# Optimization experiments

Measured on AMD Instinct MI355X. Metric: run time of the kernel, lower is better.

The kernel has to match this reference:

```python
import jax, jax.numpy as jnp
import numpy as np

HEADS = 8

def setup_inputs() -> dict:
    key = jax.random.key(0)
    k1, k2, k3 = jax.random.split(key, 3)
    dim = 256
    B, H, W = 8, 128, 128
    x = jax.random.normal(k1, (B, dim, H, W), dtype=jnp.float32)
    w_qkv = jax.random.normal(k2, (3 * dim, dim), dtype=jnp.float32) * (1.0 / np.sqrt(dim))
    b_qkv = jnp.zeros((3 * dim,), dtype=jnp.float32)
    w_out = jax.random.normal(k3, (dim, dim), dtype=jnp.float32) * (1.0 / np.sqrt(dim))
    b_out = jnp.zeros((dim,), dtype=jnp.float32)
    return {"x": x, "w_qkv": w_qkv, "b_qkv": b_qkv, "w_out": w_out, "b_out": b_out}

def reference(x, w_qkv, b_qkv, w_out, b_out):
    B, C, H, W = x.shape
    hd = C // HEADS          # head dim
    N = H * W                # spatial tokens
    # 1x1 conv == channel matmul
    qkv = jnp.einsum('oc,bchw->bohw', w_qkv, x) + b_qkv[None, :, None, None]
    q, k, v = jnp.split(qkv, 3, axis=1)
    resh = lambda t: t.reshape(B, HEADS, hd, N)  # 'b (h c) h0 w0 -> b h c (h0 w0)'
    q = jax.nn.softmax(resh(q), axis=-2)  # softmax over channel dim
    k = jax.nn.softmax(resh(k), axis=-1)  # softmax over spatial dim
    v = resh(v)
    context = jnp.einsum('bhcn,bhdn->bhcd', k, v)   # [B,h,c,d]
    out = jnp.einsum('bhcd,bhcn->bhdn', context, q) # [B,h,d,N]
    out = out.reshape(B, C, H, W)
    out = jnp.einsum('oc,bchw->bohw', w_out, out) + b_out[None, :, None, None]
    return out
```

## Files before the change

kernel.cpp:

```cpp
#include <hip/hip_runtime.h>

#define NTOK 16384

typedef short           bf16x8 __attribute__((ext_vector_type(8)));
typedef float           f32x4  __attribute__((ext_vector_type(4)));
typedef unsigned short  u16x4  __attribute__((ext_vector_type(4)));

#define WHI_OFF 0
#define WLO_OFF 98304
#define CTX_OFF 196608
#define Z_OFF   262144
#define MHI_OFF 264192
#define MLO_OFF 526336

union UB8 { unsigned u[4]; bf16x8 v; };

#define GLL16(src, dst)                                                          \
    __builtin_amdgcn_global_load_lds(                                            \
        (const __attribute__((address_space(1))) unsigned*)(src),                \
        (__attribute__((address_space(3))) unsigned*)(dst), 16, 0, 0)

__device__ __forceinline__ void split2(float v0, float v1, unsigned& hi, unsigned& lo) {
    unsigned b0 = __float_as_uint(v0), b1 = __float_as_uint(v1);
    unsigned h0 = b0 & 0xffff0000u, h1 = b1 & 0xffff0000u;
    hi = (b0 >> 16) | h1;
    float r0 = v0 - __uint_as_float(h0);
    float r1 = v1 - __uint_as_float(h1);
    lo = (__float_as_uint(r0) >> 16) | (__float_as_uint(r1) & 0xffff0000u);
}

__device__ __forceinline__ unsigned short bf16_trunc(float v) {
    return (unsigned short)(__float_as_uint(v) >> 16);
}
__device__ __forceinline__ float bf16_f(unsigned short u) {
    return __uint_as_float(((unsigned)u) << 16);
}

__global__ void splitw_k(const float* __restrict__ w,
                         unsigned short* __restrict__ whi,
                         unsigned short* __restrict__ wlo)
{
    const int gid = blockIdx.x * 256 + threadIdx.x;
    const int row = gid >> 5, c8 = gid & 31;
    const float* wp = w + row * 256 + c8 * 8;
    float4 a = *(const float4*)wp;
    float4 b = *(const float4*)(wp + 4);
    uint4 hv, lv;
    split2(a.x, a.y, hv.x, lv.x);
    split2(a.z, a.w, hv.y, lv.y);
    split2(b.x, b.y, hv.z, lv.z);
    split2(b.z, b.w, hv.w, lv.w);
    const int didx = ((row >> 4) * 8 + (c8 >> 2)) * 64 + (c8 & 3) * 16 + (row & 15);
    ((uint4*)whi)[didx] = hv;
    ((uint4*)wlo)[didx] = lv;
}

__device__ __forceinline__ void loadA(const unsigned short* __restrict__ w,
                                      int tb0, int kblk, int lane, bf16x8 a[4])
{
#pragma unroll
    for (int rt = 0; rt < 4; ++rt)
        a[rt] = *(const bf16x8*)(w + (((tb0 + rt) * 8 + kblk) * 64 + lane) * 8);
}

__device__ __forceinline__ void stageX(const float* __restrict__ xb, int k0, int n0,
                                       float* __restrict__ xsbuf, int tid)
{
    const int r = tid >> 4, s = tid & 15;
    const float* src0 = xb + (size_t)(k0 + r) * NTOK + n0 + s * 4;
    char* lds_base = (char*)xsbuf + (tid >> 6) * 1024;
    GLL16(src0, lds_base);
    GLL16(src0 + (size_t)16 * NTOK, lds_base + 4096);
}

__device__ __forceinline__ void buildB(const float* __restrict__ xs,
                                       int quad, int l16, bf16x8 bh[4], bf16x8 bl[4])
{
#pragma unroll
    for (int ct = 0; ct < 4; ++ct) {
        UB8 hu, lu;
#pragma unroll
        for (int p = 0; p < 4; ++p) {
            float v0 = xs[(quad * 8 + 2 * p) * 64 + ct * 16 + l16];
            float v1 = xs[(quad * 8 + 2 * p + 1) * 64 + ct * 16 + l16];
            split2(v0, v1, hu.u[p], lu.u[p]);
        }
        bh[ct] = hu.v; bl[ct] = lu.v;
    }
}

__device__ __forceinline__ void mfma48(f32x4 acc[4][4],
                                       const bf16x8 ah[4], const bf16x8 al[4],
                                       const bf16x8 bh[4], const bf16x8 bl[4])
{
    __builtin_amdgcn_s_setprio(1);
#pragma unroll
    for (int rt = 0; rt < 4; ++rt)
#pragma unroll
        for (int ct = 0; ct < 4; ++ct) {
            acc[rt][ct] = __builtin_amdgcn_mfma_f32_16x16x32_bf16(ah[rt], bh[ct], acc[rt][ct], 0, 0, 0);
            acc[rt][ct] = __builtin_amdgcn_mfma_f32_16x16x32_bf16(al[rt], bh[ct], acc[rt][ct], 0, 0, 0);
            acc[rt][ct] = __builtin_amdgcn_mfma_f32_16x16x32_bf16(ah[rt], bl[ct], acc[rt][ct], 0, 0, 0);
        }
    __builtin_amdgcn_s_setprio(0);
}

__launch_bounds__(256, 2)
__global__ void kv_ctx_k(const float* __restrict__ x,
                         const unsigned short* __restrict__ whi,
                         const unsigned short* __restrict__ wlo,
                         const float* __restrict__ bqkv,
                         float* __restrict__ ctxn, float* __restrict__ zsum)
{
    __shared__ __align__(16) unsigned short kvt[32768];
    float* xs0 = (float*)((char*)kvt + 32768);
    float* xs1 = (float*)((char*)kvt + 40960);

    const int tid  = threadIdx.x;
    const int wave = tid >> 6, lane = tid & 63;
    const int quad = lane >> 4, l16 = lane & 15;
    const int b = blockIdx.x >> 6, tile = blockIdx.x & 63;
    const float* xb = x + (size_t)b * 256 * NTOK;

    f32x4 cacc[2][2][2];
#pragma unroll
    for (int a0 = 0; a0 < 2; ++a0)
#pragma unroll
        for (int a1 = 0; a1 < 2; ++a1)
#pragma unroll
            for (int a2 = 0; a2 < 2; ++a2)
                cacc[a0][a1][a2] = (f32x4){0.f, 0.f, 0.f, 0.f};
    float zacc = 0.f;

    for (int chunk = 0; chunk < 4; ++chunk) {
        const int n0 = tile * 256 + chunk * 64;

        for (int half = 0; half < 2; ++half) {
            f32x4 acc[4][4];
#pragma unroll
            for (int rt = 0; rt < 4; ++rt)
#pragma unroll
                for (int ct = 0; ct < 4; ++ct) acc[rt][ct] = (f32x4){0.f, 0.f, 0.f, 0.f};

            const int tb0 = (256 + half * 256 + wave * 64) >> 4;

            stageX(xb, 0, n0, xs0, tid);
            __syncthreads();
#pragma unroll
            for (int it = 0; it < 8; ++it) {
                float* xsc = (it & 1) ? xs1 : xs0;
                float* xsn = (it & 1) ? xs0 : xs1;
                if (it < 7) stageX(xb, (it + 1) * 32, n0, xsn, tid);
                bf16x8 ah[4], al[4];
                loadA(whi, tb0, it, lane, ah);
                loadA(wlo, tb0, it, lane, al);
                bf16x8 bh[4], bl[4];
                buildB(xsc, quad, l16, bh, bl);
                mfma48(acc, ah, al, bh, bl);
                __syncthreads();
            }
#pragma unroll
            for (int rt = 0; rt < 4; ++rt)
#pragma unroll
                for (int ct = 0; ct < 4; ++ct) {
                    const int t = ct * 16 + l16;
#pragma unroll
                    for (int r = 0; r < 4; ++r) {
                        const int ch = half * 256 + wave * 64 + rt * 16 + quad * 4 + r;
                        float val = acc[rt][ct][r] + bqkv[256 + ch];
                        if (half == 0) val = __expf(val);
                        kvt[ch * 64 + (t ^ ((ch & 7) << 3))] = bf16_trunc(val);
                    }
                }
        }
        __syncthreads();

#pragma unroll
        for (int hh = 0; hh < 2; ++hh) {
            const int h = wave * 2 + hh;
#pragma unroll
            for (int ks = 0; ks < 2; ++ks) {
                const int tb = ks * 32 + quad * 8;
                bf16x8 af[2], bfr[2];
#pragma unroll
                for (int mi = 0; mi < 2; ++mi) {
                    const int ch = h * 32 + mi * 16 + l16;
                    af[mi] = *(const bf16x8*)&kvt[ch * 64 + (tb ^ ((ch & 7) << 3))];
                }
#pragma unroll
                for (int ni = 0; ni < 2; ++ni) {
                    const int ch = 256 + h * 32 + ni * 16 + l16;
                    bfr[ni] = *(const bf16x8*)&kvt[ch * 64 + (tb ^ ((ch & 7) << 3))];
                }
#pragma unroll
                for (int mi = 0; mi < 2; ++mi)
#pragma unroll
                    for (int ni = 0; ni < 2; ++ni)
                        cacc[hh][mi][ni] = __builtin_amdgcn_mfma_f32_16x16x32_bf16(af[mi], bfr[ni], cacc[hh][mi][ni], 0, 0, 0);
            }
        }
        {
            const int ch = tid;
            const int zs = (ch & 7) << 3;
#pragma unroll
            for (int t8 = 0; t8 < 8; ++t8) {
                bf16x8 v8 = *(const bf16x8*)&kvt[ch * 64 + ((t8 * 8) ^ zs)];
#pragma unroll
                for (int u = 0; u < 8; ++u) zacc += bf16_f((unsigned short)v8[u]);
            }
        }
        __syncthreads();
    }

#pragma unroll
    for (int hh = 0; hh < 2; ++hh) {
        const int h = wave * 2 + hh;
        float* cp = ctxn + ((size_t)(b * 8 + h)) * 1024;
#pragma unroll
        for (int mi = 0; mi < 2; ++mi)
#pragma unroll
            for (int ni = 0; ni < 2; ++ni)
#pragma unroll
                for (int r = 0; r < 4; ++r) {
                    const int c = mi * 16 + quad * 4 + r;
                    const int d = ni * 16 + l16;
                    atomicAdd(&cp[c * 32 + d], cacc[hh][mi][ni][r]);
                }
    }
    atomicAdd(&zsum[(b * 8 + (tid >> 5)) * 32 + (tid & 31)], zacc);
}

__global__ void build_m_k(const float* __restrict__ ctxn, const float* __restrict__ zsum,
                          const float* __restrict__ wout,
                          unsigned short* __restrict__ mhi, unsigned short* __restrict__ mlo)
{
    __shared__ float cl[1024];
    __shared__ float zl[32];
    const int b = blockIdx.x >> 3, h = blockIdx.x & 7;
    const int tid = threadIdx.x;
    if (tid < 32) zl[tid] = 1.0f / zsum[(b * 8 + h) * 32 + tid];
    __syncthreads();
    for (int i = tid; i < 1024; i += 256)
        cl[i] = ctxn[(size_t)(b * 8 + h) * 1024 + i] * zl[i >> 5];
    __syncthreads();
    const int o = tid;
    float wrow[32];
#pragma unroll
    for (int d = 0; d < 32; ++d) wrow[d] = wout[o * 256 + h * 32 + d];
    float m[32];
#pragma unroll 4
    for (int c = 0; c < 32; ++c) {
        float acc = 0.f;
#pragma unroll
        for (int d = 0; d < 32; ++d) acc += wrow[d] * cl[c * 32 + d];
        m[c] = acc;
    }
    uint4* dh = (uint4*)mhi + (size_t)b * 8192;
    uint4* dl = (uint4*)mlo + (size_t)b * 8192;
#pragma unroll
    for (int q = 0; q < 4; ++q) {
        uint4 hv, lv;
        split2(m[q * 8 + 0], m[q * 8 + 1], hv.x, lv.x);
        split2(m[q * 8 + 2], m[q * 8 + 3], hv.y, lv.y);
        split2(m[q * 8 + 4], m[q * 8 + 5], hv.z, lv.z);
        split2(m[q * 8 + 6], m[q * 8 + 7], hv.w, lv.w);
        const int di = ((o >> 4) * 8 + h) * 64 + q * 16 + (o & 15);
        dh[di] = hv; dl[di] = lv;
    }
}

__launch_bounds__(256, 2)
__global__ void final_k(const float* __restrict__ x,
                        const unsigned short* __restrict__ whi,
                        const unsigned short* __restrict__ wlo,
                        const float* __restrict__ bqkv,
                        const unsigned short* __restrict__ mhi,
                        const unsigned short* __restrict__ mlo,
                        const float* __restrict__ bout, float* __restrict__ out)
{
    __shared__ __align__(16) float qs[16384];
    unsigned short* qb = (unsigned short*)qs;
    float* xs0 = qs + 8192;
    float* xs1 = qs + 10240;
    const int tid  = threadIdx.x;
    const int wave = tid >> 6, lane = tid & 63;
    const int quad = lane >> 4, l16 = lane & 15;
    const int b = blockIdx.x >> 8, tile = blockIdx.x & 255;
    const int n0 = tile * 64;
    const float* xb = x + (size_t)b * 256 * NTOK;

    f32x4 acc[4][4];
#pragma unroll
    for (int rt = 0; rt < 4; ++rt)
#pragma unroll
        for (int ct = 0; ct < 4; ++ct) acc[rt][ct] = (f32x4){0.f, 0.f, 0.f, 0.f};

    stageX(xb, 0, n0, xs0, tid);
    __syncthreads();
#pragma unroll
    for (int it = 0; it < 8; ++it) {
        float* xsc = (it & 1) ? xs1 : xs0;
        float* xsn = (it & 1) ? xs0 : xs1;
        if (it < 7) stageX(xb, (it + 1) * 32, n0, xsn, tid);
        bf16x8 ah[4], al[4];
        loadA(whi, wave * 4, it, lane, ah);
        loadA(wlo, wave * 4, it, lane, al);
        bf16x8 bh[4], bl[4];
        buildB(xsc, quad, l16, bh, bl);
        mfma48(acc, ah, al, bh, bl);
        __syncthreads();
    }
#pragma unroll
    for (int rt = 0; rt < 4; ++rt)
#pragma unroll
        for (int ct = 0; ct < 4; ++ct) {
            const int t = ct * 16 + l16;
#pragma unroll
            for (int r = 0; r < 4; ++r) {
                const int ch = wave * 64 + rt * 16 + quad * 4 + r;
                qs[ch * 64 + t] = acc[rt][ct][r] + bqkv[ch];
            }
        }
    __syncthreads();

    unsigned qp[2][16];
#pragma unroll
    for (int rep = 0; rep < 2; ++rep) {
        const int h = (tid >> 6) + rep * 4;
        const int t = tid & 63;
        float e[32];
        float ssum = 0.f;
#pragma unroll
        for (int c = 0; c < 32; ++c) {
            e[c] = __expf(qs[(h * 32 + c) * 64 + t]);
            ssum += e[c];
        }
        const float rinv = 1.0f / ssum;
#pragma unroll
        for (int p = 0; p < 16; ++p) {
            unsigned u0 = (unsigned)bf16_trunc(e[2 * p] * rinv);
            unsigned u1 = (unsigned)bf16_trunc(e[2 * p + 1] * rinv);
            qp[rep][p] = u0 | (u1 << 16);
        }
    }
    __syncthreads();
#pragma unroll
    for (int rep = 0; rep < 2; ++rep) {
        const int h = (tid >> 6) + rep * 4;
        const int t = tid & 63;
        const int s = (t & 7) << 3;
#pragma unroll
        for (int g = 0; g < 4; ++g) {
            UB8 w8;
#pragma unroll
            for (int p = 0; p < 4; ++p) w8.u[p] = qp[rep][g * 4 + p];
            *(bf16x8*)&qb[t * 256 + ((h * 32 + g * 8) ^ s)] = w8.v;
        }
    }
    __syncthreads();

#pragma unroll
    for (int rt = 0; rt < 4; ++rt)
#pragma unroll
        for (int ct = 0; ct < 4; ++ct) acc[rt][ct] = (f32x4){0.f, 0.f, 0.f, 0.f};
    const unsigned short* mhb = mhi + (size_t)b * 65536;
    const unsigned short* mlb = mlo + (size_t)b * 65536;

    bf16x8 mah[2][4], mal[2][4];
    loadA(mhb, wave * 4, 0, lane, mah[0]);
    loadA(mlb, wave * 4, 0, lane, mal[0]);
#pragma unroll
    for (int it = 0; it < 8; ++it) {
        const int cb = it & 1, nb = cb ^ 1;
        if (it < 7) {
            loadA(mhb, wave * 4, it + 1, lane, mah[nb]);
            loadA(mlb, wave * 4, it + 1, lane, mal[nb]);
        }
        bf16x8 bq[4];
#pragma unroll
        for (int ct = 0; ct < 4; ++ct) {
            const int t = ct * 16 + l16;
            const int s = (t & 7) << 3;
            bq[ct] = *(const bf16x8*)&qb[t * 256 + ((it * 32 + quad * 8) ^ s)];
        }
        __builtin_amdgcn_s_setprio(1);
#pragma unroll
        for (int rt = 0; rt < 4; ++rt)
#pragma unroll
            for (int ct = 0; ct < 4; ++ct) {
                acc[rt][ct] = __builtin_amdgcn_mfma_f32_16x16x32_bf16(mah[cb][rt], bq[ct], acc[rt][ct], 0, 0, 0);
                acc[rt][ct] = __builtin_amdgcn_mfma_f32_16x16x32_bf16(mal[cb][rt], bq[ct], acc[rt][ct], 0, 0, 0);
            }
        __builtin_amdgcn_s_setprio(0);
    }

    float* ob = out + (size_t)b * 256 * NTOK;
#pragma unroll
    for (int rt = 0; rt < 4; ++rt)
#pragma unroll
        for (int ct = 0; ct < 4; ++ct) {
            const int t = ct * 16 + l16;
#pragma unroll
            for (int r = 0; r < 4; ++r) {
                const int o = wave * 64 + rt * 16 + quad * 4 + r;
                ob[(size_t)o * NTOK + n0 + t] = acc[rt][ct][r] + bout[o];
            }
        }
}

extern "C" void kernel_launch(void* const* d_in, const int* in_sizes, int n_in,
                              void* d_out, int out_size, void* d_ws, size_t ws_size,
                              hipStream_t stream)
{
    (void)in_sizes; (void)n_in; (void)out_size; (void)ws_size;
    const float* x    = (const float*)d_in[0];
    const float* wqkv = (const float*)d_in[1];
    const float* bqkv = (const float*)d_in[2];
    const float* wout = (const float*)d_in[3];
    const float* bout = (const float*)d_in[4];
    float* out = (float*)d_out;
    float* ws  = (float*)d_ws;

    unsigned short* whi = (unsigned short*)(ws + WHI_OFF);
    unsigned short* wlo = (unsigned short*)(ws + WLO_OFF);
    float*          ctx = ws + CTX_OFF;
    float*          zs  = ws + Z_OFF;
    unsigned short* mhi = (unsigned short*)(ws + MHI_OFF);
    unsigned short* mlo = (unsigned short*)(ws + MLO_OFF);

    hipMemsetAsync(ctx, 0, (65536 + 2048) * sizeof(float), stream);
    splitw_k<<<96, 256, 0, stream>>>(wqkv, whi, wlo);
    kv_ctx_k<<<512, 256, 0, stream>>>(x, whi, wlo, bqkv, ctx, zs);
    build_m_k<<<64, 256, 0, stream>>>(ctx, zs, wout, mhi, mlo);
    final_k<<<2048, 256, 0, stream>>>(x, whi, wlo, bqkv, mhi, mlo, bout, out);
}
```

Measured before the change: 419.5 us.

## Fuse K/V projection passes and deepen X staging to four-buffer pipeline

In kv_ctx_k the K and V projections now share one pass over x per chunk, so each x tile is staged and converted into B fragments once instead of twice. Both kernels now stage x through a four-slot ring of LDS buffers kept three tiles ahead, using explicit vmcnt waits and a bare barrier in place of a full __syncthreads after every step. This is meant to halve x traffic in the KV kernel and hide global-load latency better. In exchange, KV accumulator registers double, which may hurt occupancy or cause spills, and the hand-written vmcnt counts must match how many loads stageX actually issues.

```diff
diff --git a/kernel.cpp b/kernel.cpp
--- a/kernel.cpp
+++ b/kernel.cpp
@@ -4,7 +4,6 @@
 
 typedef short           bf16x8 __attribute__((ext_vector_type(8)));
 typedef float           f32x4  __attribute__((ext_vector_type(4)));
-typedef unsigned short  u16x4  __attribute__((ext_vector_type(4)));
 
 #define WHI_OFF 0
 #define WLO_OFF 98304
@@ -34,6 +33,12 @@
 }
 __device__ __forceinline__ float bf16_f(unsigned short u) {
     return __uint_as_float(((unsigned)u) << 16);
+}
+
+__device__ __forceinline__ void wait_stage(int it) {
+    if (it <= 5)      asm volatile("s_waitcnt vmcnt(4)" ::: "memory");
+    else if (it == 6) asm volatile("s_waitcnt vmcnt(2)" ::: "memory");
+    else              asm volatile("s_waitcnt vmcnt(0)" ::: "memory");
 }
 
 __global__ void splitw_k(const float* __restrict__ w,
@@ -113,8 +118,7 @@
                          float* __restrict__ ctxn, float* __restrict__ zsum)
 {
     __shared__ __align__(16) unsigned short kvt[32768];
-    float* xs0 = (float*)((char*)kvt + 32768);
-    float* xs1 = (float*)((char*)kvt + 40960);
+#define XSBUF(i) ((float*)((char*)kvt + 32768 + (i) * 8192))
 
     const int tid  = threadIdx.x;
     const int wave = tid >> 6, lane = tid & 63;
@@ -135,44 +139,52 @@
     for (int chunk = 0; chunk < 4; ++chunk) {
         const int n0 = tile * 256 + chunk * 64;
 
-        for (int half = 0; half < 2; ++half) {
-            f32x4 acc[4][4];
-#pragma unroll
-            for (int rt = 0; rt < 4; ++rt)
-#pragma unroll
-                for (int ct = 0; ct < 4; ++ct) acc[rt][ct] = (f32x4){0.f, 0.f, 0.f, 0.f};
-
-            const int tb0 = (256 + half * 256 + wave * 64) >> 4;
-
-            stageX(xb, 0, n0, xs0, tid);
-            __syncthreads();
-#pragma unroll
-            for (int it = 0; it < 8; ++it) {
-                float* xsc = (it & 1) ? xs1 : xs0;
-                float* xsn = (it & 1) ? xs0 : xs1;
-                if (it < 7) stageX(xb, (it + 1) * 32, n0, xsn, tid);
-                bf16x8 ah[4], al[4];
-                loadA(whi, tb0, it, lane, ah);
-                loadA(wlo, tb0, it, lane, al);
-                bf16x8 bh[4], bl[4];
-                buildB(xsc, quad, l16, bh, bl);
-                mfma48(acc, ah, al, bh, bl);
-                __syncthreads();
-            }
-#pragma unroll
-            for (int rt = 0; rt < 4; ++rt)
-#pragma unroll
-                for (int ct = 0; ct < 4; ++ct) {
-                    const int t = ct * 16 + l16;
-#pragma unroll
-                    for (int r = 0; r < 4; ++r) {
-                        const int ch = half * 256 + wave * 64 + rt * 16 + quad * 4 + r;
-                        float val = acc[rt][ct][r] + bqkv[256 + ch];
-                        if (half == 0) val = __expf(val);
-                        kvt[ch * 64 + (t ^ ((ch & 7) << 3))] = bf16_trunc(val);
-                    }
+        f32x4 accK[4][4], accV[4][4];
+#pragma unroll
+        for (int rt = 0; rt < 4; ++rt)
+#pragma unroll
+            for (int ct = 0; ct < 4; ++ct) {
+                accK[rt][ct] = (f32x4){0.f, 0.f, 0.f, 0.f};
+                accV[rt][ct] = (f32x4){0.f, 0.f, 0.f, 0.f};
+            }
+
+        stageX(xb,  0, n0, XSBUF(0), tid);
+        stageX(xb, 32, n0, XSBUF(1), tid);
+        stageX(xb, 64, n0, XSBUF(2), tid);
+
+#pragma unroll
+        for (int it = 0; it < 8; ++it) {
+            wait_stage(it);
+            __builtin_amdgcn_s_barrier();
+            bf16x8 ahk[4], alk[4], ahv[4], alv[4];
+            loadA(whi, 16 + wave * 4, it, lane, ahk);
+            loadA(wlo, 16 + wave * 4, it, lane, alk);
+            loadA(whi, 32 + wave * 4, it, lane, ahv);
+            loadA(wlo, 32 + wave * 4, it, lane, alv);
+            if (it < 5) stageX(xb, (it + 3) * 32, n0, XSBUF((it + 3) & 3), tid);
+            __builtin_amdgcn_sched_barrier(0);
+            bf16x8 bh[4], bl[4];
+            buildB(XSBUF(it & 3), quad, l16, bh, bl);
+            mfma48(accK, ahk, alk, bh, bl);
+            mfma48(accV, ahv, alv, bh, bl);
+        }
+        __syncthreads();
+
+#pragma unroll
+        for (int rt = 0; rt < 4; ++rt)
+#pragma unroll
+            for (int ct = 0; ct < 4; ++ct) {
+                const int t = ct * 16 + l16;
+#pragma unroll
+                for (int r = 0; r < 4; ++r) {
+                    const int chk = wave * 64 + rt * 16 + quad * 4 + r;
+                    float vk = accK[rt][ct][r] + bqkv[256 + chk];
+                    kvt[chk * 64 + (t ^ ((chk & 7) << 3))] = bf16_trunc(__expf(vk));
+                    const int chv = 256 + chk;
+                    float vv = accV[rt][ct][r] + bqkv[256 + chv];
+                    kvt[chv * 64 + (t ^ ((chv & 7) << 3))] = bf16_trunc(vv);
                 }
-        }
+            }
         __syncthreads();
 
 #pragma unroll
@@ -228,6 +240,7 @@
                 }
     }
     atomicAdd(&zsum[(b * 8 + (tid >> 5)) * 32 + (tid & 31)], zacc);
+#undef XSBUF
 }
 
 __global__ void build_m_k(const float* __restrict__ ctxn, const float* __restrict__ zsum,
@@ -280,8 +293,7 @@
 {
     __shared__ __align__(16) float qs[16384];
     unsigned short* qb = (unsigned short*)qs;
-    float* xs0 = qs + 8192;
-    float* xs1 = qs + 10240;
+#define FSBUF(i) ((float*)((char*)qs + 32768 + (i) * 8192))
     const int tid  = threadIdx.x;
     const int wave = tid >> 6, lane = tid & 63;
     const int quad = lane >> 4, l16 = lane & 15;
@@ -295,21 +307,24 @@
 #pragma unroll
         for (int ct = 0; ct < 4; ++ct) acc[rt][ct] = (f32x4){0.f, 0.f, 0.f, 0.f};
 
-    stageX(xb, 0, n0, xs0, tid);
-    __syncthreads();
+    stageX(xb,  0, n0, FSBUF(0), tid);
+    stageX(xb, 32, n0, FSBUF(1), tid);
+    stageX(xb, 64, n0, FSBUF(2), tid);
 #pragma unroll
     for (int it = 0; it < 8; ++it) {
-        float* xsc = (it & 1) ? xs1 : xs0;
-        float* xsn = (it & 1) ? xs0 : xs1;
-        if (it < 7) stageX(xb, (it + 1) * 32, n0, xsn, tid);
+        wait_stage(it);
+        __builtin_amdgcn_s_barrier();
         bf16x8 ah[4], al[4];
         loadA(whi, wave * 4, it, lane, ah);
         loadA(wlo, wave * 4, it, lane, al);
+        if (it < 5) stageX(xb, (it + 3) * 32, n0, FSBUF((it + 3) & 3), tid);
+        __builtin_amdgcn_sched_barrier(0);
         bf16x8 bh[4], bl[4];
-        buildB(xsc, quad, l16, bh, bl);
+        buildB(FSBUF(it & 3), quad, l16, bh, bl);
         mfma48(acc, ah, al, bh, bl);
-        __syncthreads();
-    }
+    }
+    __syncthreads();
+
 #pragma unroll
     for (int rt = 0; rt < 4; ++rt)
 #pragma unroll
@@ -406,6 +421,7 @@
                 ob[(size_t)o * NTOK + n0 + t] = acc[rt][ct][r] + bout[o];
             }
         }
+#undef FSBUF
 }
 
 extern "C" void kernel_launch(void* const* d_in, const int* in_sizes, int n_in,
```

Result: slower. 820.7 us (+95.6%).

## Pre-split x into swizzled bf16 hi/lo planes once, reused by both GEMM kernels

Applied to the files above, without the earlier changes.

Adds a kernel that converts x once into bf16 hi/lo planes in a swizzled tile layout in workspace. Both the K/V-context kernel and the final kernel then stage these planes with global_load_lds and read B fragments directly, instead of re-splitting fp32 x per k-step. This removes the duplicated split ALU work and LDS gather, but adds a full extra pass writing and re-reading a bf16x2 copy of x, the same size as x itself. The new path is used only when the workspace is large enough; otherwise the old fp32 path runs.

```diff
diff --git a/kernel.cpp b/kernel.cpp
--- a/kernel.cpp
+++ b/kernel.cpp
@@ -12,6 +12,8 @@
 #define Z_OFF   262144
 #define MHI_OFF 264192
 #define MLO_OFF 526336
+#define XSP_OFF 788480
+#define WS_NEED_BYTES 137371648ull
 
 union UB8 { unsigned u[4]; bf16x8 v; };
 
@@ -89,6 +91,62 @@
     }
 }
 
+
+__global__ void splitx_k(const float* __restrict__ x,
+                         unsigned short* __restrict__ xsp)
+{
+    __shared__ __align__(16) float sl[2048];
+    const int tid = threadIdx.x;
+    const int b = blockIdx.x >> 8, T = blockIdx.x & 255;
+    const float* xb = x + (size_t)b * 256 * NTOK;
+    unsigned short* xpb = xsp + (size_t)b * (256 * 8 * 2 * 2048);
+    const int t = ((tid >> 6) << 4) + ((tid & 63) >> 2);
+    const int g = tid & 3;
+    const int idx = t * 32 + ((g ^ ((t >> 1) & 3)) * 8);
+    for (int K = 0; K < 8; ++K) {
+        stageX(xb, K * 32, T * 64, sl, tid);
+        __syncthreads();
+        float v[8];
+#pragma unroll
+        for (int i = 0; i < 8; ++i) v[i] = sl[(g * 8 + i) * 64 + t];
+        uint4 hv, lv;
+        split2(v[0], v[1], hv.x, lv.x);
+        split2(v[2], v[3], hv.y, lv.y);
+        split2(v[4], v[5], hv.z, lv.z);
+        split2(v[6], v[7], hv.w, lv.w);
+        unsigned short* blk = xpb + (size_t)(T * 8 + K) * 4096;
+        *(uint4*)(blk + idx) = hv;
+        *(uint4*)(blk + 2048 + idx) = lv;
+        __syncthreads();
+    }
+}
+
+__device__ __forceinline__ void stageS(const unsigned short* __restrict__ xpb,
+                                       int Tt, int kstep, char* slot, int tid)
+{
+    const int wb = (tid >> 6) * 1024;
+    const int lb = wb + (tid & 63) * 16;
+#pragma unroll
+    for (int ks = 0; ks < 2; ++ks)
+#pragma unroll
+        for (int p = 0; p < 2; ++p) {
+            const char* src = (const char*)(xpb + (size_t)(Tt * 8 + kstep * 2 + ks) * 4096
+                                                + p * 2048);
+            GLL16(src + lb, slot + ks * 8192 + p * 4096 + wb);
+        }
+}
+
+__device__ __forceinline__ void loadBspl(const char* plane, int quad, int l16,
+                                         bf16x8 bfrag[4])
+{
+    const unsigned short* pl = (const unsigned short*)plane;
+#pragma unroll
+    for (int ct = 0; ct < 4; ++ct) {
+        const int t = ct * 16 + l16;
+        bfrag[ct] = *(const bf16x8*)(pl + t * 32 + ((quad ^ ((t >> 1) & 3)) * 8));
+    }
+}
+
 __device__ __forceinline__ void mfma48(f32x4 acc[4][4],
                                        const bf16x8 ah[4], const bf16x8 al[4],
                                        const bf16x8 bh[4], const bf16x8 bl[4])
@@ -105,22 +163,25 @@
     __builtin_amdgcn_s_setprio(0);
 }
 
+template<bool PS>
 __launch_bounds__(256, 2)
 __global__ void kv_ctx_k(const float* __restrict__ x,
+                         const unsigned short* __restrict__ xsp,
                          const unsigned short* __restrict__ whi,
                          const unsigned short* __restrict__ wlo,
                          const float* __restrict__ bqkv,
                          float* __restrict__ ctxn, float* __restrict__ zsum)
 {
     __shared__ __align__(16) unsigned short kvt[32768];
-    float* xs0 = (float*)((char*)kvt + 32768);
-    float* xs1 = (float*)((char*)kvt + 40960);
+#define SLOT(i) ((char*)kvt + 32768 + (i) * 16384)
+#define XF(i)   ((float*)((char*)kvt + 32768 + (i) * 8192))
 
     const int tid  = threadIdx.x;
     const int wave = tid >> 6, lane = tid & 63;
     const int quad = lane >> 4, l16 = lane & 15;
     const int b = blockIdx.x >> 6, tile = blockIdx.x & 63;
     const float* xb = x + (size_t)b * 256 * NTOK;
+    const unsigned short* xpb = xsp + (size_t)b * (256 * 8 * 2 * 2048);
 
     f32x4 cacc[2][2][2];
 #pragma unroll
@@ -134,6 +195,7 @@
 
     for (int chunk = 0; chunk < 4; ++chunk) {
         const int n0 = tile * 256 + chunk * 64;
+        const int Tt = tile * 4 + chunk;
 
         for (int half = 0; half < 2; ++half) {
             f32x4 acc[4][4];
@@ -142,23 +204,44 @@
 #pragma unroll
                 for (int ct = 0; ct < 4; ++ct) acc[rt][ct] = (f32x4){0.f, 0.f, 0.f, 0.f};
 
-            const int tb0 = (256 + half * 256 + wave * 64) >> 4;
-
-            stageX(xb, 0, n0, xs0, tid);
-            __syncthreads();
-#pragma unroll
-            for (int it = 0; it < 8; ++it) {
-                float* xsc = (it & 1) ? xs1 : xs0;
-                float* xsn = (it & 1) ? xs0 : xs1;
-                if (it < 7) stageX(xb, (it + 1) * 32, n0, xsn, tid);
-                bf16x8 ah[4], al[4];
-                loadA(whi, tb0, it, lane, ah);
-                loadA(wlo, tb0, it, lane, al);
-                bf16x8 bh[4], bl[4];
-                buildB(xsc, quad, l16, bh, bl);
-                mfma48(acc, ah, al, bh, bl);
+            const int tb0 = 16 + half * 16 + wave * 4;
+
+            if constexpr (PS) {
+                stageS(xpb, Tt, 0, SLOT(0), tid);
                 __syncthreads();
-            }
+#pragma unroll
+                for (int st = 0; st < 4; ++st) {
+                    char* cur = SLOT(st & 1);
+                    if (st < 3) stageS(xpb, Tt, st + 1, SLOT((st + 1) & 1), tid);
+#pragma unroll
+                    for (int ks = 0; ks < 2; ++ks) {
+                        const int kblk = st * 2 + ks;
+                        bf16x8 ah[4], al[4], bh[4], bl[4];
+                        loadA(whi, tb0, kblk, lane, ah);
+                        loadA(wlo, tb0, kblk, lane, al);
+                        loadBspl(cur + ks * 8192, quad, l16, bh);
+                        loadBspl(cur + ks * 8192 + 4096, quad, l16, bl);
+                        mfma48(acc, ah, al, bh, bl);
+                    }
+                    __syncthreads();
+                }
+            } else {
+                stageX(xb, 0, n0, XF(0), tid);
+                __syncthreads();
+#pragma unroll
+                for (int it = 0; it < 8; ++it) {
+                    float* xsc = XF(it & 1);
+                    if (it < 7) stageX(xb, (it + 1) * 32, n0, XF((it + 1) & 1), tid);
+                    bf16x8 ah[4], al[4];
+                    loadA(whi, tb0, it, lane, ah);
+                    loadA(wlo, tb0, it, lane, al);
+                    bf16x8 bh[4], bl[4];
+                    buildB(xsc, quad, l16, bh, bl);
+                    mfma48(acc, ah, al, bh, bl);
+                    __syncthreads();
+                }
+            }
+
 #pragma unroll
             for (int rt = 0; rt < 4; ++rt)
 #pragma unroll
@@ -228,6 +311,8 @@
                 }
     }
     atomicAdd(&zsum[(b * 8 + (tid >> 5)) * 32 + (tid & 31)], zacc);
+#undef SLOT
+#undef XF
 }
 
 __global__ void build_m_k(const float* __restrict__ ctxn, const float* __restrict__ zsum,
@@ -269,8 +354,10 @@
     }
 }
 
+template<bool PS>
 __launch_bounds__(256, 2)
 __global__ void final_k(const float* __restrict__ x,
+                        const unsigned short* __restrict__ xsp,
                         const unsigned short* __restrict__ whi,
                         const unsigned short* __restrict__ wlo,
                         const float* __restrict__ bqkv,
@@ -280,14 +367,15 @@
 {
     __shared__ __align__(16) float qs[16384];
     unsigned short* qb = (unsigned short*)qs;
-    float* xs0 = qs + 8192;
-    float* xs1 = qs + 10240;
+#define FSLOT(i) ((char*)qs + 32768 + (i) * 16384)
+#define FXF(i)   ((float*)((char*)qs + 32768 + (i) * 8192))
     const int tid  = threadIdx.x;
     const int wave = tid >> 6, lane = tid & 63;
     const int quad = lane >> 4, l16 = lane & 15;
     const int b = blockIdx.x >> 8, tile = blockIdx.x & 255;
     const int n0 = tile * 64;
     const float* xb = x + (size_t)b * 256 * NTOK;
+    const unsigned short* xpb = xsp + (size_t)b * (256 * 8 * 2 * 2048);
 
     f32x4 acc[4][4];
 #pragma unroll
@@ -295,21 +383,42 @@
 #pragma unroll
         for (int ct = 0; ct < 4; ++ct) acc[rt][ct] = (f32x4){0.f, 0.f, 0.f, 0.f};
 
-    stageX(xb, 0, n0, xs0, tid);
-    __syncthreads();
-#pragma unroll
-    for (int it = 0; it < 8; ++it) {
-        float* xsc = (it & 1) ? xs1 : xs0;
-        float* xsn = (it & 1) ? xs0 : xs1;
-        if (it < 7) stageX(xb, (it + 1) * 32, n0, xsn, tid);
-        bf16x8 ah[4], al[4];
-        loadA(whi, wave * 4, it, lane, ah);
-        loadA(wlo, wave * 4, it, lane, al);
-        bf16x8 bh[4], bl[4];
-        buildB(xsc, quad, l16, bh, bl);
-        mfma48(acc, ah, al, bh, bl);
+    if constexpr (PS) {
+        stageS(xpb, tile, 0, FSLOT(0), tid);
         __syncthreads();
-    }
+#pragma unroll
+        for (int st = 0; st < 4; ++st) {
+            char* cur = FSLOT(st & 1);
+            if (st < 3) stageS(xpb, tile, st + 1, FSLOT((st + 1) & 1), tid);
+#pragma unroll
+            for (int ks = 0; ks < 2; ++ks) {
+                const int kblk = st * 2 + ks;
+                bf16x8 ah[4], al[4], bh[4], bl[4];
+                loadA(whi, wave * 4, kblk, lane, ah);
+                loadA(wlo, wave * 4, kblk, lane, al);
+                loadBspl(cur + ks * 8192, quad, l16, bh);
+                loadBspl(cur + ks * 8192 + 4096, quad, l16, bl);
+                mfma48(acc, ah, al, bh, bl);
+            }
+            __syncthreads();
+        }
+    } else {
+        stageX(xb, 0, n0, FXF(0), tid);
+        __syncthreads();
+#pragma unroll
+        for (int it = 0; it < 8; ++it) {
+            float* xsc = FXF(it & 1);
+            if (it < 7) stageX(xb, (it + 1) * 32, n0, FXF((it + 1) & 1), tid);
+            bf16x8 ah[4], al[4];
+            loadA(whi, wave * 4, it, lane, ah);
+            loadA(wlo, wave * 4, it, lane, al);
+            bf16x8 bh[4], bl[4];
+            buildB(xsc, quad, l16, bh, bl);
+            mfma48(acc, ah, al, bh, bl);
+            __syncthreads();
+        }
+    }
+
 #pragma unroll
     for (int rt = 0; rt < 4; ++rt)
 #pragma unroll
@@ -406,13 +515,15 @@
                 ob[(size_t)o * NTOK + n0 + t] = acc[rt][ct][r] + bout[o];
             }
         }
+#undef FSLOT
+#undef FXF
 }
 
 extern "C" void kernel_launch(void* const* d_in, const int* in_sizes, int n_in,
                               void* d_out, int out_size, void* d_ws, size_t ws_size,
                               hipStream_t stream)
 {
-    (void)in_sizes; (void)n_in; (void)out_size; (void)ws_size;
+    (void)in_sizes; (void)n_in; (void)out_size;
     const float* x    = (const float*)d_in[0];
     const float* wqkv = (const float*)d_in[1];
     const float* bqkv = (const float*)d_in[2];
@@ -427,10 +538,20 @@
     float*          zs  = ws + Z_OFF;
     unsigned short* mhi = (unsigned short*)(ws + MHI_OFF);
     unsigned short* mlo = (unsigned short*)(ws + MLO_OFF);
+    unsigned short* xsp = (unsigned short*)(ws + XSP_OFF);
+
+    const bool presplit = ws_size >= WS_NEED_BYTES;
 
     hipMemsetAsync(ctx, 0, (65536 + 2048) * sizeof(float), stream);
     splitw_k<<<96, 256, 0, stream>>>(wqkv, whi, wlo);
-    kv_ctx_k<<<512, 256, 0, stream>>>(x, whi, wlo, bqkv, ctx, zs);
-    build_m_k<<<64, 256, 0, stream>>>(ctx, zs, wout, mhi, mlo);
-    final_k<<<2048, 256, 0, stream>>>(x, whi, wlo, bqkv, mhi, mlo, bout, out);
-}
+    if (presplit) {
+        splitx_k<<<2048, 256, 0, stream>>>(x, xsp);
+        kv_ctx_k<true><<<512, 256, 0, stream>>>(x, xsp, whi, wlo, bqkv, ctx, zs);
+        build_m_k<<<64, 256, 0, stream>>>(ctx, zs, wout, mhi, mlo);
+        final_k<true><<<2048, 256, 0, stream>>>(x, xsp, whi, wlo, bqkv, mhi, mlo, bout, out);
+    } else {
+        kv_ctx_k<false><<<512, 256, 0, stream>>>(x, nullptr, whi, wlo, bqkv, ctx, zs);
+        build_m_k<<<64, 256, 0, stream>>>(ctx, zs, wout, mhi, mlo);
+        final_k<false><<<2048, 256, 0, stream>>>(x, nullptr, whi, wlo, bqkv, mhi, mlo, bout, out);
+    }
+}
```

New measurement: 448.9 us. +7.0%, slower.
